# Kernel optimization log

Measured on AMD Instinct MI355X. Metric: run time of the kernel, lower is better.

The kernel has to match this reference:

```python
import jax, jax.numpy as jnp
import numpy as np

B, S, D = 4, 2048, 1024
H, HD = 16, 64  # num_head, head_dim


def setup_inputs() -> dict:
    key = jax.random.key(0)
    k0, k1, k2, k3, k4 = jax.random.split(key, 5)
    scale = 1.0 / np.sqrt(D)
    return {
        "x": jax.random.normal(k0, (B, S, D), dtype=jnp.float32),
        "Wq": jax.random.normal(k1, (D, H * HD), dtype=jnp.float32) * scale,
        "Wk": jax.random.normal(k2, (D, H * HD), dtype=jnp.float32) * scale,
        "Wv": jax.random.normal(k3, (D, H * HD), dtype=jnp.float32) * scale,
        "Wo": jax.random.normal(k4, (H * HD, H * HD), dtype=jnp.float32) * scale,
    }


def reference(x, Wq, Wk, Wv, Wo):
    b, s, _ = x.shape
    # projections -> [b, h, s, hd]
    q = (x @ Wq).reshape(b, s, H, HD).transpose(0, 2, 1, 3)
    k = (x @ Wk).reshape(b, s, H, HD).transpose(0, 2, 1, 3)
    v = (x @ Wv).reshape(b, s, H, HD).transpose(0, 2, 1, 3)
    # scaled scores [b, h, s, s]
    scores = jnp.einsum("bhqd,bhkd->bhqk", q, k) / np.sqrt(HD).astype(np.float32)
    causal = jnp.triu(jnp.ones((s, s), dtype=bool), k=1)  # True above diagonal
    scores = jnp.where(causal, -jnp.inf, scores)
    att = jax.nn.softmax(scores, axis=-1)
    # dropout p=0.0 -> identity
    out = jnp.einsum("bhqk,bhkd->bqhd", att, v).reshape(b, s, H * HD)
    return out @ Wo
```

## Files before the change

### kernel.cpp

```cpp
#include <hip/hip_runtime.h>


typedef __attribute__((ext_vector_type(8))) short short8_t;
typedef __attribute__((ext_vector_type(4))) short short4_t;
typedef __attribute__((ext_vector_type(4))) float float4_t;

constexpr int Bz = 4, Sq = 2048, Dm = 1024, NH = 16, HD = 64;

#define GLOAD_LDS16(g, l)                                                      \
  __builtin_amdgcn_global_load_lds(                                            \
      (const __attribute__((address_space(1))) unsigned int*)(g),              \
      (__attribute__((address_space(3))) unsigned int*)(l), 16, 0, 0)

__device__ __forceinline__ unsigned short f2bf(float f) {
  unsigned u = __builtin_bit_cast(unsigned, f);
  u += 0x7fffu + ((u >> 16) & 1u);
  return (unsigned short)(u >> 16);
}

__device__ __forceinline__ float exp2_fast(float x) {
#if __has_builtin(__builtin_amdgcn_exp2f)
  return __builtin_amdgcn_exp2f(x);
#else
  return exp2f(x);
#endif
}

__device__ __forceinline__ float m3(float a, float b, float c) {
  return fmaxf(fmaxf(a, b), c);
}

__global__ __launch_bounds__(256) void cast_x_kernel(const float* __restrict__ x,
                                                     unsigned short* __restrict__ xb) {
  size_t i = (size_t)blockIdx.x * 256 + threadIdx.x;
  float4 v = ((const float4*)x)[i];
  ushort4 o;
  o.x = f2bf(v.x); o.y = f2bf(v.y); o.z = f2bf(v.z); o.w = f2bf(v.w);
  ((ushort4*)xb)[i] = o;
}

__global__ __launch_bounds__(256) void transpose_w_kernel(
    const float* __restrict__ Wq, const float* __restrict__ Wk,
    const float* __restrict__ Wv, const float* __restrict__ Wo,
    unsigned short* __restrict__ wqT, unsigned short* __restrict__ wkT,
    unsigned short* __restrict__ wvT, unsigned short* __restrict__ woT) {
  __shared__ float tile[64][65];
  int zz = blockIdx.z;
  const float* W = zz == 0 ? Wq : (zz == 1 ? Wk : (zz == 2 ? Wv : Wo));
  unsigned short* WT = zz == 0 ? wqT : (zz == 1 ? wkT : (zz == 2 ? wvT : woT));
  int n0 = blockIdx.x * 64, k0 = blockIdx.y * 64;
  int tx = threadIdx.x & 63, ty = threadIdx.x >> 6;
#pragma unroll
  for (int i = 0; i < 16; ++i) {
    int r = i * 4 + ty;
    tile[r][tx] = W[(size_t)(k0 + r) * Dm + n0 + tx];
  }
  __syncthreads();
#pragma unroll
  for (int i = 0; i < 16; ++i) {
    int r = i * 4 + ty;
    WT[(size_t)(n0 + r) * Dm + k0 + tx] = f2bf(tile[tx][r]);
  }
}

#define SBAR do { __builtin_amdgcn_sched_barrier(0); __builtin_amdgcn_s_barrier(); } while (0)
#define VMW(n_) asm volatile("s_waitcnt vmcnt(" #n_ ")" ::: "memory")

#define STG_A(buf_, h_, kt_) do {                                              \
  GLOAD_LDS16(gA + (size_t)(mloc0 + (h_) * 64) * Dm + (kt_) * 64 + csA,        \
              smA + (buf_) * 16384 + (h_) * 8192 + tid * 8);                   \
  GLOAD_LDS16(gA + (size_t)(mloc1 + (h_) * 64) * Dm + (kt_) * 64 + csA,        \
              smA + (buf_) * 16384 + (h_) * 8192 + 4096 + tid * 8);            \
} while (0)
#define STG_B(buf_, h_, kt_) do {                                              \
  GLOAD_LDS16(gB + (size_t)(nloc0 + (h_) * 32) * Dm + (kt_) * 64 + csA,        \
              smB + (buf_) * 16384 + (h_) * 8192 + tid * 8);                   \
  GLOAD_LDS16(gB + (size_t)(nloc1 + (h_) * 32) * Dm + (kt_) * 64 + csA,        \
              smB + (buf_) * 16384 + (h_) * 8192 + 4096 + tid * 8);            \
} while (0)
#define LDA_(buf_, mh_) do {                                                   \
  _Pragma("unroll") for (int i_ = 0; i_ < 4; ++i_) {                           \
    const unsigned short* p_ = smA + (buf_) * 16384 + (mh_) * 8192 + aoff + i_ * 1024; \
    a[i_][0] = *(const short8_t*)(p_ + csw0);                                  \
    a[i_][1] = *(const short8_t*)(p_ + csw1);                                  \
  }                                                                            \
} while (0)
#define LDB_(dst_, buf_, nh_) do {                                             \
  _Pragma("unroll") for (int j_ = 0; j_ < 2; ++j_) {                           \
    const unsigned short* p_ = smB + (buf_) * 16384 + (nh_) * 8192 + boff + j_ * 1024; \
    dst_[j_][0] = *(const short8_t*)(p_ + csw0);                               \
    dst_[j_][1] = *(const short8_t*)(p_ + csw1);                               \
  }                                                                            \
} while (0)
#define MF_(ioff_, breg_, joff_) do {                                          \
  __builtin_amdgcn_s_setprio(1);                                               \
  _Pragma("unroll") for (int i_ = 0; i_ < 4; ++i_)                             \
  _Pragma("unroll") for (int j_ = 0; j_ < 2; ++j_) {                           \
    acc[(ioff_) + i_][(joff_) + j_] = __builtin_amdgcn_mfma_f32_16x16x32_bf16( \
        a[i_][0], breg_[j_][0], acc[(ioff_) + i_][(joff_) + j_], 0, 0, 0);     \
    acc[(ioff_) + i_][(joff_) + j_] = __builtin_amdgcn_mfma_f32_16x16x32_bf16( \
        a[i_][1], breg_[j_][1], acc[(ioff_) + i_][(joff_) + j_], 0, 0, 0);     \
  }                                                                            \
  __builtin_amdgcn_s_setprio(0);                                               \
} while (0)

__device__ __forceinline__ void gemm256_mainloop(
    const unsigned short* __restrict__ A, const unsigned short* __restrict__ BT,
    int m0, int n0, unsigned short* smA, unsigned short* smB,
    float4_t acc[8][4]) {
  const int tid = threadIdx.x;
  const int lane = tid & 63, lr = lane & 15, quad = lane >> 4;
  const int wid = tid >> 6, wm = wid >> 2, wn = wid & 3;
  const int aoff = (wm * 64 + lr) * 64;
  const int boff = (wn * 32 + lr) * 64;
  const int csw0 = (quad ^ (lr & 7)) * 8;
  const int csw1 = csw0 ^ 32;
  const int lrow0 = tid >> 3;
  const int csA = ((tid & 7) ^ (lrow0 & 7)) * 8;
  const int mloc0 = lrow0, mloc1 = lrow0 + 128;
  const int nloc0 = (lrow0 >> 5) * 64 + (lrow0 & 31);
  const int nloc1 = nloc0 + 128;
  const unsigned short* gA = A + (size_t)m0 * Dm;
  const unsigned short* gB = BT + (size_t)n0 * Dm;

  short8_t a[4][2], b0[2][2], b1[2][2];

  STG_A(0, 0, 0); STG_A(0, 1, 0); STG_B(0, 0, 0); STG_B(0, 1, 0);
  STG_A(1, 0, 1); STG_B(1, 0, 1); STG_B(1, 1, 1);
  VMW(6);
  SBAR;

#pragma unroll 1
  for (int T = 0; T < 7; ++T) {
    const int t1 = 2 * T + 1, t2 = 2 * T + 2, t3 = 2 * T + 3;
    LDA_(0, 0); LDB_(b0, 0, 0); STG_A(1, 1, t1); SBAR; MF_(0, b0, 0); SBAR;
    LDB_(b1, 0, 1);             STG_A(0, 0, t2); SBAR; MF_(0, b1, 2); SBAR;
    LDA_(0, 1);                 STG_B(0, 0, t2); SBAR; MF_(4, b0, 0); SBAR;
                                STG_B(0, 1, t2); SBAR; MF_(4, b1, 2); VMW(6); SBAR;
    LDA_(1, 0); LDB_(b0, 1, 0); STG_A(0, 1, t2); SBAR; MF_(0, b0, 0); SBAR;
    LDB_(b1, 1, 1);             STG_A(1, 0, t3); SBAR; MF_(0, b1, 2); SBAR;
    LDA_(1, 1);                 STG_B(1, 0, t3); SBAR; MF_(4, b0, 0); SBAR;
                                STG_B(1, 1, t3); SBAR; MF_(4, b1, 2); VMW(6); SBAR;
  }
  LDA_(0, 0); LDB_(b0, 0, 0); STG_A(1, 1, 15); SBAR; MF_(0, b0, 0); SBAR;
  LDB_(b1, 0, 1);                              SBAR; MF_(0, b1, 2); SBAR;
  LDA_(0, 1);                                  SBAR; MF_(4, b0, 0); SBAR;
                                               SBAR; MF_(4, b1, 2); VMW(0); SBAR;
  LDA_(1, 0); LDB_(b0, 1, 0);                  SBAR; MF_(0, b0, 0); SBAR;
  LDB_(b1, 1, 1);                              SBAR; MF_(0, b1, 2); SBAR;
  LDA_(1, 1);                                  SBAR; MF_(4, b0, 0); SBAR;
                                               SBAR; MF_(4, b1, 2);
}

__global__ __launch_bounds__(512, 2) void gemm_qkv_kernel(
    const unsigned short* __restrict__ xb,
    const unsigned short* __restrict__ wqT, const unsigned short* __restrict__ wkT,
    const unsigned short* __restrict__ wvT,
    unsigned short* __restrict__ qb, unsigned short* __restrict__ kb,
    unsigned short* __restrict__ vt) {
  __shared__ unsigned short smA[32768];
  __shared__ unsigned short smB[32768];
  int lin = (int)blockIdx.x;
  int logical = (lin & 7) * 48 + (lin >> 3);
  int bx = logical & 3;
  int by = (logical >> 2) & 31;
  int bz = logical >> 7;
  const unsigned short* WT = bz == 0 ? wqT : (bz == 1 ? wkT : wvT);
  unsigned short* outb = bz == 0 ? qb : (bz == 1 ? kb : vt);
  bool isV = bz == 2;
  float qscale = (bz == 0) ? 0.18033688011112042f : 1.0f;
  int m0 = by * 256, n0 = bx * 256;
  float4_t z = {0.f, 0.f, 0.f, 0.f};
  float4_t acc[8][4];
#pragma unroll
  for (int i = 0; i < 8; ++i)
#pragma unroll
    for (int j = 0; j < 4; ++j) acc[i][j] = z;
  gemm256_mainloop(xb, WT, m0, n0, smA, smB, acc);

  const int lane = threadIdx.x & 63, lr = lane & 15, quad = lane >> 4;
  const int wid = threadIdx.x >> 6, wm = wid >> 2, wn = wid & 3;
  const int mb = m0 + wm * 128 + quad * 4;
  const int nb = n0 + wn * 64 + lr;
  if (isV) {
#pragma unroll
    for (int ai = 0; ai < 8; ++ai)
#pragma unroll
      for (int bj = 0; bj < 4; ++bj) {
        int m = mb + (ai >> 2) * 64 + (ai & 3) * 16;
        int n = nb + (bj >> 1) * 32 + (bj & 1) * 16;
        int b = m >> 11, s = m & (Sq - 1);
        int h = n >> 6, hd = n & (HD - 1);
        ushort4 pk;
        pk.x = f2bf(acc[ai][bj][0]); pk.y = f2bf(acc[ai][bj][1]);
        pk.z = f2bf(acc[ai][bj][2]); pk.w = f2bf(acc[ai][bj][3]);
        *(ushort4*)(outb + (((size_t)b * NH + h) * HD + hd) * Sq + s) = pk;
      }
  } else {
#pragma unroll
    for (int ai = 0; ai < 8; ++ai)
#pragma unroll
      for (int bj = 0; bj < 4; ++bj)
#pragma unroll
        for (int r = 0; r < 4; ++r) {
          int m = mb + (ai >> 2) * 64 + (ai & 3) * 16 + r;
          int n = nb + (bj >> 1) * 32 + (bj & 1) * 16;
          int b = m >> 11, s = m & (Sq - 1);
          int h = n >> 6, hd = n & (HD - 1);
          outb[(((size_t)b * NH + h) * Sq + s) * HD + hd] = f2bf(acc[ai][bj][r] * qscale);
        }
  }
}

__global__ __launch_bounds__(512, 2) void gemm_out_kernel(
    const unsigned short* __restrict__ ao, const unsigned short* __restrict__ woT,
    float* __restrict__ out) {
  __shared__ unsigned short smA[32768];
  __shared__ unsigned short smB[32768];
  int lin = (int)blockIdx.x;
  int logical = (lin & 7) * 16 + (lin >> 3);
  int bx = logical & 3;
  int by = logical >> 2;
  int m0 = by * 256, n0 = bx * 256;
  float4_t z = {0.f, 0.f, 0.f, 0.f};
  float4_t acc[8][4];
#pragma unroll
  for (int i = 0; i < 8; ++i)
#pragma unroll
    for (int j = 0; j < 4; ++j) acc[i][j] = z;
  gemm256_mainloop(ao, woT, m0, n0, smA, smB, acc);

  const int lane = threadIdx.x & 63, lr = lane & 15, quad = lane >> 4;
  const int wid = threadIdx.x >> 6, wm = wid >> 2, wn = wid & 3;
  const int mb = m0 + wm * 128 + quad * 4;
  const int nb = n0 + wn * 64 + lr;
#pragma unroll
  for (int ai = 0; ai < 8; ++ai)
#pragma unroll
    for (int bj = 0; bj < 4; ++bj)
#pragma unroll
      for (int r = 0; r < 4; ++r) {
        int m = mb + (ai >> 2) * 64 + (ai & 3) * 16 + r;
        int n = nb + (bj >> 1) * 32 + (bj & 1) * 16;
        out[(size_t)m * Dm + n] = acc[ai][bj][r];
      }
}

__global__ __launch_bounds__(256) void attn_kernel(
    const unsigned short* __restrict__ qbuf, const unsigned short* __restrict__ kbuf,
    const unsigned short* __restrict__ vtbuf, unsigned short* __restrict__ ao) {
  __shared__ unsigned short lk[2 * 64 * 64];
  __shared__ unsigned short lv[2 * 64 * 64];
  int tid = threadIdx.x;
  int bh = blockIdx.x;
  int ti = 31 - (int)blockIdx.y;
  int wave = tid >> 6, lane = tid & 63;
  int lcol = lane & 15, quad = lane >> 4;
  int lc7 = lcol & 7;
  const unsigned short* Q = qbuf + (size_t)bh * Sq * HD;
  const unsigned short* K = kbuf + (size_t)bh * Sq * HD;
  const unsigned short* Vt = vtbuf + (size_t)bh * HD * Sq;
  int b = bh >> 4, h = bh & 15;
  float4_t z = {0.f, 0.f, 0.f, 0.f};

  const int r0 = tid >> 3;
  const int sgk = (tid & 7) ^ (r0 & 7);
  const unsigned short* kg = K + (size_t)r0 * HD + sgk * 8;
  const int kdst = tid * 8;

  const int w0 = (tid & 7) * 2;
  const int xa = r0 & 15;
  const int d0 = w0 ^ xa;
  const unsigned short* vsrc = Vt + (size_t)r0 * Sq + w0 * 4;
  const int vdst = r0 * 64 + d0 * 4;

  const int koff0 = (quad ^ lc7) * 8;
  const int koff1 = ((quad | 4) ^ lc7) * 8;
  int voff[4];
#pragma unroll
  for (int s4 = 0; s4 < 4; ++s4) voff[s4] = ((s4 * 4 + quad) ^ lcol) * 4;

  unsigned short* lkc = lk;
  unsigned short* lkn = lk + 4096;
  unsigned short* lvc = lv;
  unsigned short* lvn = lv + 4096;

  int q0w = ti * 64 + wave * 16;
  int q_global = q0w + lcol;
  short8_t qf0 = *(const short8_t*)(Q + (size_t)(q0w + lcol) * HD + quad * 8);
  short8_t qf1 = *(const short8_t*)(Q + (size_t)(q0w + lcol) * HD + 32 + quad * 8);
  float m_i = -INFINITY, l_i = 0.f;
  float4_t o[4];
#pragma unroll
  for (int f = 0; f < 4; ++f) o[f] = z;

  {
    GLOAD_LDS16(kg, lkc + kdst);
    GLOAD_LDS16(kg + (size_t)32 * HD, lkc + 2048 + kdst);
    short4_t a0 = *(const short4_t*)(vsrc);
    short4_t a1 = *(const short4_t*)(vsrc + 4);
    short4_t b0 = *(const short4_t*)(vsrc + (size_t)32 * Sq);
    short4_t b1 = *(const short4_t*)(vsrc + (size_t)32 * Sq + 4);
    *(short4_t*)(lvc + vdst) = a0;
    *(short4_t*)(lvc + (vdst ^ 4)) = a1;
    *(short4_t*)(lvc + vdst + 2048) = b0;
    *(short4_t*)(lvc + (vdst ^ 4) + 2048) = b1;
  }
  __syncthreads();

  int nkt = ti + 1;
  for (int kt = 0; kt < nkt; ++kt) {
    bool has_next = (kt + 1 < nkt);
    short4_t a0, a1, b0, b1;
    if (has_next) {
      const unsigned short* vs = vsrc + (size_t)(kt + 1) * 64;
      a0 = *(const short4_t*)(vs);
      a1 = *(const short4_t*)(vs + 4);
      b0 = *(const short4_t*)(vs + (size_t)32 * Sq);
      b1 = *(const short4_t*)(vs + (size_t)32 * Sq + 4);
      const unsigned short* kgn = kg + (size_t)(kt + 1) * 64 * HD;
      GLOAD_LDS16(kgn, lkn + kdst);
      GLOAD_LDS16(kgn + (size_t)32 * HD, lkn + 2048 + kdst);
    }

    float s[16];
#pragma unroll
    for (int s4 = 0; s4 < 4; ++s4) {
      const unsigned short* kr = lkc + (s4 * 16 + lcol) * 64;
      short8_t kf0 = *(const short8_t*)(kr + koff0);
      short8_t kf1 = *(const short8_t*)(kr + koff1);
      float4_t st = z;
      st = __builtin_amdgcn_mfma_f32_16x16x32_bf16(kf0, qf0, st, 0, 0, 0);
      st = __builtin_amdgcn_mfma_f32_16x16x32_bf16(kf1, qf1, st, 0, 0, 0);
#pragma unroll
      for (int r = 0; r < 4; ++r) s[s4 * 4 + r] = st[r];
    }
    if (kt == ti) {
      int key0 = kt * 64;
#pragma unroll
      for (int s4 = 0; s4 < 4; ++s4)
#pragma unroll
        for (int r = 0; r < 4; ++r)
          if (key0 + s4 * 16 + quad * 4 + r > q_global) s[s4 * 4 + r] = -INFINITY;
    }

    float ta = m3(s[0], s[1], s[2]);
    float tb = m3(s[3], s[4], s[5]);
    float tc = m3(s[6], s[7], s[8]);
    float td = m3(s[9], s[10], s[11]);
    float te = m3(s[12], s[13], s[14]);
    float tmax = m3(ta, tb, tc);
    tmax = m3(tmax, td, te);
    tmax = fmaxf(tmax, s[15]);
    tmax = fmaxf(tmax, __shfl_xor(tmax, 16, 64));
    tmax = fmaxf(tmax, __shfl_xor(tmax, 32, 64));

    if (__any(tmax > m_i + 8.f)) {
      float m_new = fmaxf(m_i, tmax);
      float alpha = exp2_fast(m_i - m_new);
      l_i *= alpha;
      m_i = m_new;
      float at[4];
#pragma unroll
      for (int r = 0; r < 4; ++r) at[r] = __shfl(alpha, quad * 4 + r, 64);
#pragma unroll
      for (int f = 0; f < 4; ++f)
#pragma unroll
        for (int r = 0; r < 4; ++r) o[f][r] *= at[r];
    }

    float psum = 0.f;
    short4_t pf[4];
#pragma unroll
    for (int s4 = 0; s4 < 4; ++s4) {
      float p0 = exp2_fast(s[s4 * 4 + 0] - m_i);
      float p1 = exp2_fast(s[s4 * 4 + 1] - m_i);
      float p2 = exp2_fast(s[s4 * 4 + 2] - m_i);
      float p3 = exp2_fast(s[s4 * 4 + 3] - m_i);
      psum += (p0 + p1) + (p2 + p3);
      unsigned lo, hi;
      asm("v_cvt_pk_bf16_f32 %0, %1, %2" : "=v"(lo) : "v"(p0), "v"(p1));
      asm("v_cvt_pk_bf16_f32 %0, %1, %2" : "=v"(hi) : "v"(p2), "v"(p3));
      uint2 packed;
      packed.x = lo;
      packed.y = hi;
      pf[s4] = __builtin_bit_cast(short4_t, packed);
    }
    psum += __shfl_xor(psum, 16, 64);
    psum += __shfl_xor(psum, 32, 64);
    l_i += psum;

    if (has_next) {
      *(short4_t*)(lvn + vdst) = a0;
      *(short4_t*)(lvn + (vdst ^ 4)) = a1;
      *(short4_t*)(lvn + vdst + 2048) = b0;
      *(short4_t*)(lvn + (vdst ^ 4) + 2048) = b1;
    }

#pragma unroll
    for (int f = 0; f < 4; ++f) {
      const unsigned short* vr = lvc + (f * 16 + lcol) * 64;
#pragma unroll
      for (int s4 = 0; s4 < 4; ++s4) {
        short4_t vf = *(const short4_t*)(vr + voff[s4]);
        o[f] = __builtin_amdgcn_mfma_f32_16x16x16bf16_1k(pf[s4], vf, o[f], 0, 0, 0);
      }
    }

    __syncthreads();
    unsigned short* t;
    t = lkc; lkc = lkn; lkn = t;
    t = lvc; lvc = lvn; lvn = t;
  }

  float lt[4];
#pragma unroll
  for (int r = 0; r < 4; ++r) lt[r] = 1.f / __shfl(l_i, quad * 4 + r, 64);
#pragma unroll
  for (int f = 0; f < 4; ++f)
#pragma unroll
    for (int r = 0; r < 4; ++r) {
      int q = q0w + quad * 4 + r;
      int hd = f * 16 + lcol;
      ao[((size_t)b * Sq + q) * (NH * HD) + h * HD + hd] = f2bf(o[f][r] * lt[r]);
    }
}

extern "C" void kernel_launch(void* const* d_in, const int* in_sizes, int n_in,
                              void* d_out, int out_size, void* d_ws, size_t ws_size,
                              hipStream_t stream) {
  const float* x = (const float*)d_in[0];
  const float* Wq = (const float*)d_in[1];
  const float* Wk = (const float*)d_in[2];
  const float* Wv = (const float*)d_in[3];
  const float* Wo = (const float*)d_in[4];
  float* out = (float*)d_out;

  char* ws = (char*)d_ws;
  size_t off = 0;
  auto carve = [&](size_t bytes) {
    void* p = ws + off;
    off += (bytes + 255) & ~(size_t)255;
    return p;
  };
  const size_t xe = (size_t)Bz * Sq * Dm;
  const size_t we = (size_t)Dm * Dm;
  unsigned short* xb = (unsigned short*)carve(xe * 2);
  unsigned short* wqT = (unsigned short*)carve(we * 2);
  unsigned short* wkT = (unsigned short*)carve(we * 2);
  unsigned short* wvT = (unsigned short*)carve(we * 2);
  unsigned short* woT = (unsigned short*)carve(we * 2);
  unsigned short* qb = (unsigned short*)carve(xe * 2);
  unsigned short* kb = (unsigned short*)carve(xe * 2);
  unsigned short* vt = (unsigned short*)carve(xe * 2);
  unsigned short* ao = (unsigned short*)carve(xe * 2);
  (void)ws_size;

  cast_x_kernel<<<xe / 4 / 256, 256, 0, stream>>>(x, xb);
  transpose_w_kernel<<<dim3(16, 16, 4), 256, 0, stream>>>(Wq, Wk, Wv, Wo,
                                                          wqT, wkT, wvT, woT);
  gemm_qkv_kernel<<<384, 512, 0, stream>>>(xb, wqT, wkT, wvT, qb, kb, vt);
  attn_kernel<<<dim3(Bz * NH, 32), 256, 0, stream>>>(qb, kb, vt, ao);
  gemm_out_kernel<<<128, 512, 0, stream>>>(ao, woT, out);
}
```

Baseline: 262.8 us.

## Shrink GEMM tiles to 128x256 to double block count

Both projection GEMMs switch from 256x256 to 128x256 block tiles. This doubles the grid (768 and 256 blocks) so the 256 CUs stay busier, and it halves the accumulator registers and A-tile LDS. The software pipeline and staging macros are rewritten around the new tile shape and fragment layout. The cost is lower arithmetic intensity per block and more re-reads of the B tile across blocks.

After: 249.6 us. 5.0% less time.

```diff
diff --git a/kernel.cpp b/kernel.cpp
--- a/kernel.cpp
+++ b/kernel.cpp
@@ -66,90 +66,81 @@
 #define SBAR do { __builtin_amdgcn_sched_barrier(0); __builtin_amdgcn_s_barrier(); } while (0)
 #define VMW(n_) asm volatile("s_waitcnt vmcnt(" #n_ ")" ::: "memory")
 
-#define STG_A(buf_, h_, kt_) do {                                              \
-  GLOAD_LDS16(gA + (size_t)(mloc0 + (h_) * 64) * Dm + (kt_) * 64 + csA,        \
-              smA + (buf_) * 16384 + (h_) * 8192 + tid * 8);                   \
-  GLOAD_LDS16(gA + (size_t)(mloc1 + (h_) * 64) * Dm + (kt_) * 64 + csA,        \
-              smA + (buf_) * 16384 + (h_) * 8192 + 4096 + tid * 8);            \
+#define STGA2(buf_, kt_) do {                                                  \
+  GLOAD_LDS16(gA + (size_t)lrow * Dm + (kt_) * 64 + csA,                       \
+              smA + (buf_) * 8192 + tid * 8);                                  \
+  GLOAD_LDS16(gA + (size_t)(lrow + 64) * Dm + (kt_) * 64 + csA,                \
+              smA + (buf_) * 8192 + 4096 + tid * 8);                           \
 } while (0)
-#define STG_B(buf_, h_, kt_) do {                                              \
-  GLOAD_LDS16(gB + (size_t)(nloc0 + (h_) * 32) * Dm + (kt_) * 64 + csA,        \
-              smB + (buf_) * 16384 + (h_) * 8192 + tid * 8);                   \
-  GLOAD_LDS16(gB + (size_t)(nloc1 + (h_) * 32) * Dm + (kt_) * 64 + csA,        \
-              smB + (buf_) * 16384 + (h_) * 8192 + 4096 + tid * 8);            \
+#define STGB4(buf_, kt_) do {                                                  \
+  GLOAD_LDS16(gB + (size_t)lrow * Dm + (kt_) * 64 + csA,                       \
+              smB + (buf_) * 16384 + tid * 8);                                 \
+  GLOAD_LDS16(gB + (size_t)(lrow + 64) * Dm + (kt_) * 64 + csA,                \
+              smB + (buf_) * 16384 + 4096 + tid * 8);                          \
+  GLOAD_LDS16(gB + (size_t)(lrow + 128) * Dm + (kt_) * 64 + csA,               \
+              smB + (buf_) * 16384 + 8192 + tid * 8);                          \
+  GLOAD_LDS16(gB + (size_t)(lrow + 192) * Dm + (kt_) * 64 + csA,               \
+              smB + (buf_) * 16384 + 12288 + tid * 8);                         \
 } while (0)
-#define LDA_(buf_, mh_) do {                                                   \
+#define LDA8(buf_) do {                                                        \
   _Pragma("unroll") for (int i_ = 0; i_ < 4; ++i_) {                           \
-    const unsigned short* p_ = smA + (buf_) * 16384 + (mh_) * 8192 + aoff + i_ * 1024; \
+    const unsigned short* p_ = smA + (buf_) * 8192 + aoff + i_ * 1024;         \
     a[i_][0] = *(const short8_t*)(p_ + csw0);                                  \
     a[i_][1] = *(const short8_t*)(p_ + csw1);                                  \
   }                                                                            \
 } while (0)
-#define LDB_(dst_, buf_, nh_) do {                                             \
+#define LDB4(dst_, buf_, jh_) do {                                             \
   _Pragma("unroll") for (int j_ = 0; j_ < 2; ++j_) {                           \
-    const unsigned short* p_ = smB + (buf_) * 16384 + (nh_) * 8192 + boff + j_ * 1024; \
+    const unsigned short* p_ =                                                 \
+        smB + (buf_) * 16384 + boff + ((jh_) * 2 + j_) * 1024;                 \
     dst_[j_][0] = *(const short8_t*)(p_ + csw0);                               \
     dst_[j_][1] = *(const short8_t*)(p_ + csw1);                               \
   }                                                                            \
 } while (0)
-#define MF_(ioff_, breg_, joff_) do {                                          \
+#define MF16(breg_, joff_) do {                                                \
   __builtin_amdgcn_s_setprio(1);                                               \
   _Pragma("unroll") for (int i_ = 0; i_ < 4; ++i_)                             \
   _Pragma("unroll") for (int j_ = 0; j_ < 2; ++j_) {                           \
-    acc[(ioff_) + i_][(joff_) + j_] = __builtin_amdgcn_mfma_f32_16x16x32_bf16( \
-        a[i_][0], breg_[j_][0], acc[(ioff_) + i_][(joff_) + j_], 0, 0, 0);     \
-    acc[(ioff_) + i_][(joff_) + j_] = __builtin_amdgcn_mfma_f32_16x16x32_bf16( \
-        a[i_][1], breg_[j_][1], acc[(ioff_) + i_][(joff_) + j_], 0, 0, 0);     \
+    acc[i_][(joff_) + j_] = __builtin_amdgcn_mfma_f32_16x16x32_bf16(           \
+        a[i_][0], breg_[j_][0], acc[i_][(joff_) + j_], 0, 0, 0);               \
+    acc[i_][(joff_) + j_] = __builtin_amdgcn_mfma_f32_16x16x32_bf16(           \
+        a[i_][1], breg_[j_][1], acc[i_][(joff_) + j_], 0, 0, 0);               \
   }                                                                            \
   __builtin_amdgcn_s_setprio(0);                                               \
 } while (0)
 
-__device__ __forceinline__ void gemm256_mainloop(
+__device__ __forceinline__ void gemm128x256_mainloop(
     const unsigned short* __restrict__ A, const unsigned short* __restrict__ BT,
-    int m0, int n0, unsigned short* smA, unsigned short* smB,
-    float4_t acc[8][4]) {
+    int m0, int n0, unsigned short* smA, unsigned short* smB, float4_t acc[4][4]) {
   const int tid = threadIdx.x;
   const int lane = tid & 63, lr = lane & 15, quad = lane >> 4;
   const int wid = tid >> 6, wm = wid >> 2, wn = wid & 3;
   const int aoff = (wm * 64 + lr) * 64;
-  const int boff = (wn * 32 + lr) * 64;
+  const int boff = (wn * 64 + lr) * 64;
   const int csw0 = (quad ^ (lr & 7)) * 8;
   const int csw1 = csw0 ^ 32;
-  const int lrow0 = tid >> 3;
-  const int csA = ((tid & 7) ^ (lrow0 & 7)) * 8;
-  const int mloc0 = lrow0, mloc1 = lrow0 + 128;
-  const int nloc0 = (lrow0 >> 5) * 64 + (lrow0 & 31);
-  const int nloc1 = nloc0 + 128;
+  const int lrow = tid >> 3;
+  const int csA = ((tid & 7) ^ (lrow & 7)) * 8;
   const unsigned short* gA = A + (size_t)m0 * Dm;
   const unsigned short* gB = BT + (size_t)n0 * Dm;
 
-  short8_t a[4][2], b0[2][2], b1[2][2];
-
-  STG_A(0, 0, 0); STG_A(0, 1, 0); STG_B(0, 0, 0); STG_B(0, 1, 0);
-  STG_A(1, 0, 1); STG_B(1, 0, 1); STG_B(1, 1, 1);
-  VMW(6);
-  SBAR;
+  short8_t a[4][2], bA[2][2], bB[2][2];
+
+  STGA2(0, 0); STGB4(0, 0); STGA2(1, 1);
+  VMW(2); SBAR;
 
 #pragma unroll 1
   for (int T = 0; T < 7; ++T) {
     const int t1 = 2 * T + 1, t2 = 2 * T + 2, t3 = 2 * T + 3;
-    LDA_(0, 0); LDB_(b0, 0, 0); STG_A(1, 1, t1); SBAR; MF_(0, b0, 0); SBAR;
-    LDB_(b1, 0, 1);             STG_A(0, 0, t2); SBAR; MF_(0, b1, 2); SBAR;
-    LDA_(0, 1);                 STG_B(0, 0, t2); SBAR; MF_(4, b0, 0); SBAR;
-                                STG_B(0, 1, t2); SBAR; MF_(4, b1, 2); VMW(6); SBAR;
-    LDA_(1, 0); LDB_(b0, 1, 0); STG_A(0, 1, t2); SBAR; MF_(0, b0, 0); SBAR;
-    LDB_(b1, 1, 1);             STG_A(1, 0, t3); SBAR; MF_(0, b1, 2); SBAR;
-    LDA_(1, 1);                 STG_B(1, 0, t3); SBAR; MF_(4, b0, 0); SBAR;
-                                STG_B(1, 1, t3); SBAR; MF_(4, b1, 2); VMW(6); SBAR;
-  }
-  LDA_(0, 0); LDB_(b0, 0, 0); STG_A(1, 1, 15); SBAR; MF_(0, b0, 0); SBAR;
-  LDB_(b1, 0, 1);                              SBAR; MF_(0, b1, 2); SBAR;
-  LDA_(0, 1);                                  SBAR; MF_(4, b0, 0); SBAR;
-                                               SBAR; MF_(4, b1, 2); VMW(0); SBAR;
-  LDA_(1, 0); LDB_(b0, 1, 0);                  SBAR; MF_(0, b0, 0); SBAR;
-  LDB_(b1, 1, 1);                              SBAR; MF_(0, b1, 2); SBAR;
-  LDA_(1, 1);                                  SBAR; MF_(4, b0, 0); SBAR;
-                                               SBAR; MF_(4, b1, 2);
+    LDA8(0); LDB4(bA, 0, 0); STGB4(1, t1); SBAR; MF16(bA, 0); SBAR;
+    LDB4(bB, 0, 1); STGA2(0, t2); SBAR; MF16(bB, 2); VMW(2); SBAR;
+    LDA8(1); LDB4(bA, 1, 0); STGB4(0, t2); SBAR; MF16(bA, 0); SBAR;
+    LDB4(bB, 1, 1); STGA2(1, t3); SBAR; MF16(bB, 2); VMW(2); SBAR;
+  }
+  LDA8(0); LDB4(bA, 0, 0); STGB4(1, 15); SBAR; MF16(bA, 0); SBAR;
+  LDB4(bB, 0, 1); SBAR; MF16(bB, 2); VMW(0); SBAR;
+  LDA8(1); LDB4(bA, 1, 0); SBAR; MF16(bA, 0); SBAR;
+  LDB4(bB, 1, 1); SBAR; MF16(bB, 2);
 }
 
 __global__ __launch_bounds__(512, 2) void gemm_qkv_kernel(
@@ -158,37 +149,37 @@
     const unsigned short* __restrict__ wvT,
     unsigned short* __restrict__ qb, unsigned short* __restrict__ kb,
     unsigned short* __restrict__ vt) {
-  __shared__ unsigned short smA[32768];
-  __shared__ unsigned short smB[32768];
+  __shared__ unsigned short smA[2 * 8192];
+  __shared__ unsigned short smB[2 * 16384];
   int lin = (int)blockIdx.x;
-  int logical = (lin & 7) * 48 + (lin >> 3);
+  int logical = (lin & 7) * 96 + (lin >> 3);
   int bx = logical & 3;
-  int by = (logical >> 2) & 31;
-  int bz = logical >> 7;
+  int by = (logical >> 2) & 63;
+  int bz = logical >> 8;
   const unsigned short* WT = bz == 0 ? wqT : (bz == 1 ? wkT : wvT);
   unsigned short* outb = bz == 0 ? qb : (bz == 1 ? kb : vt);
   bool isV = bz == 2;
   float qscale = (bz == 0) ? 0.18033688011112042f : 1.0f;
-  int m0 = by * 256, n0 = bx * 256;
+  int m0 = by * 128, n0 = bx * 256;
   float4_t z = {0.f, 0.f, 0.f, 0.f};
-  float4_t acc[8][4];
-#pragma unroll
-  for (int i = 0; i < 8; ++i)
+  float4_t acc[4][4];
+#pragma unroll
+  for (int i = 0; i < 4; ++i)
 #pragma unroll
     for (int j = 0; j < 4; ++j) acc[i][j] = z;
-  gemm256_mainloop(xb, WT, m0, n0, smA, smB, acc);
+  gemm128x256_mainloop(xb, WT, m0, n0, smA, smB, acc);
 
   const int lane = threadIdx.x & 63, lr = lane & 15, quad = lane >> 4;
   const int wid = threadIdx.x >> 6, wm = wid >> 2, wn = wid & 3;
-  const int mb = m0 + wm * 128 + quad * 4;
+  const int mb = m0 + wm * 64 + quad * 4;
   const int nb = n0 + wn * 64 + lr;
   if (isV) {
 #pragma unroll
-    for (int ai = 0; ai < 8; ++ai)
+    for (int ai = 0; ai < 4; ++ai)
 #pragma unroll
       for (int bj = 0; bj < 4; ++bj) {
-        int m = mb + (ai >> 2) * 64 + (ai & 3) * 16;
-        int n = nb + (bj >> 1) * 32 + (bj & 1) * 16;
+        int m = mb + ai * 16;
+        int n = nb + bj * 16;
         int b = m >> 11, s = m & (Sq - 1);
         int h = n >> 6, hd = n & (HD - 1);
         ushort4 pk;
@@ -198,13 +189,13 @@
       }
   } else {
 #pragma unroll
-    for (int ai = 0; ai < 8; ++ai)
+    for (int ai = 0; ai < 4; ++ai)
 #pragma unroll
       for (int bj = 0; bj < 4; ++bj)
 #pragma unroll
         for (int r = 0; r < 4; ++r) {
-          int m = mb + (ai >> 2) * 64 + (ai & 3) * 16 + r;
-          int n = nb + (bj >> 1) * 32 + (bj & 1) * 16;
+          int m = mb + ai * 16 + r;
+          int n = nb + bj * 16;
           int b = m >> 11, s = m & (Sq - 1);
           int h = n >> 6, hd = n & (HD - 1);
           outb[(((size_t)b * NH + h) * Sq + s) * HD + hd] = f2bf(acc[ai][bj][r] * qscale);
@@ -215,33 +206,33 @@
 __global__ __launch_bounds__(512, 2) void gemm_out_kernel(
     const unsigned short* __restrict__ ao, const unsigned short* __restrict__ woT,
     float* __restrict__ out) {
-  __shared__ unsigned short smA[32768];
-  __shared__ unsigned short smB[32768];
+  __shared__ unsigned short smA[2 * 8192];
+  __shared__ unsigned short smB[2 * 16384];
   int lin = (int)blockIdx.x;
-  int logical = (lin & 7) * 16 + (lin >> 3);
+  int logical = (lin & 7) * 32 + (lin >> 3);
   int bx = logical & 3;
   int by = logical >> 2;
-  int m0 = by * 256, n0 = bx * 256;
+  int m0 = by * 128, n0 = bx * 256;
   float4_t z = {0.f, 0.f, 0.f, 0.f};
-  float4_t acc[8][4];
-#pragma unroll
-  for (int i = 0; i < 8; ++i)
+  float4_t acc[4][4];
+#pragma unroll
+  for (int i = 0; i < 4; ++i)
 #pragma unroll
     for (int j = 0; j < 4; ++j) acc[i][j] = z;
-  gemm256_mainloop(ao, woT, m0, n0, smA, smB, acc);
+  gemm128x256_mainloop(ao, woT, m0, n0, smA, smB, acc);
 
   const int lane = threadIdx.x & 63, lr = lane & 15, quad = lane >> 4;
   const int wid = threadIdx.x >> 6, wm = wid >> 2, wn = wid & 3;
-  const int mb = m0 + wm * 128 + quad * 4;
+  const int mb = m0 + wm * 64 + quad * 4;
   const int nb = n0 + wn * 64 + lr;
 #pragma unroll
-  for (int ai = 0; ai < 8; ++ai)
+  for (int ai = 0; ai < 4; ++ai)
 #pragma unroll
     for (int bj = 0; bj < 4; ++bj)
 #pragma unroll
       for (int r = 0; r < 4; ++r) {
-        int m = mb + (ai >> 2) * 64 + (ai & 3) * 16 + r;
-        int n = nb + (bj >> 1) * 32 + (bj & 1) * 16;
+        int m = mb + ai * 16 + r;
+        int n = nb + bj * 16;
         out[(size_t)m * Dm + n] = acc[ai][bj][r];
       }
 }
@@ -459,7 +450,7 @@
   cast_x_kernel<<<xe / 4 / 256, 256, 0, stream>>>(x, xb);
   transpose_w_kernel<<<dim3(16, 16, 4), 256, 0, stream>>>(Wq, Wk, Wv, Wo,
                                                           wqT, wkT, wvT, woT);
-  gemm_qkv_kernel<<<384, 512, 0, stream>>>(xb, wqT, wkT, wvT, qb, kb, vt);
+  gemm_qkv_kernel<<<768, 512, 0, stream>>>(xb, wqT, wkT, wvT, qb, kb, vt);
   attn_kernel<<<dim3(Bz * NH, 32), 256, 0, stream>>>(qb, kb, vt, ao);
-  gemm_out_kernel<<<128, 512, 0, stream>>>(ao, woT, out);
-}
+  gemm_out_kernel<<<256, 512, 0, stream>>>(ao, woT, out);
+}
```
